# Kernel optimization log

Hardware: AMD Instinct MI355X
Metric: run time of the kernel (lower is better)

## Reference

```python
import jax, jax.numpy as jnp
import numpy as np

B, H, VOCAB, STEPS = 256, 512, 100, 200  # TEXT_MAX_LEN - 1 = 200
SOS_IDX = 0  # char2idx['<SOS>'] == 0 (first entry of chars list)


def setup_inputs() -> dict:
    key = jax.random.key(0)
    ks = jax.random.split(key, 8)
    s = 0.05  # keep gates/tanh away from saturation, like trained-weight scale
    return {
        "feat": jax.random.normal(ks[0], (B, H), jnp.float32),          # resnet pooler_output
        "embed_table": jax.random.normal(ks[1], (VOCAB, H), jnp.float32) * s,
        "w_ih": jax.random.normal(ks[2], (3 * H, H), jnp.float32) * s,   # torch weight_ih_l0
        "w_hh": jax.random.normal(ks[3], (3 * H, H), jnp.float32) * s,   # torch weight_hh_l0
        "b_ih": jax.random.normal(ks[4], (3 * H,), jnp.float32) * s,
        "b_hh": jax.random.normal(ks[5], (3 * H,), jnp.float32) * s,
        "proj_w": jax.random.normal(ks[6], (VOCAB, H), jnp.float32) * s,
        "proj_b": jax.random.normal(ks[7], (VOCAB,), jnp.float32) * s,
    }


def _gru_cell(x, h, w_ih, w_hh, b_ih, b_hh):
    # torch GRU cell: gates ordered [r, z, n]
    gi = x @ w_ih.T + b_ih          # [B, 3H]
    gh = h @ w_hh.T + b_hh          # [B, 3H]
    i_r, i_z, i_n = jnp.split(gi, 3, axis=-1)
    h_r, h_z, h_n = jnp.split(gh, 3, axis=-1)
    r = jax.nn.sigmoid(i_r + h_r)
    z = jax.nn.sigmoid(i_z + h_z)
    n = jnp.tanh(i_n + r * h_n)
    return (1.0 - z) * n + z * h


def reference(feat, embed_table, w_ih, w_hh, b_ih, b_hh, proj_w, proj_b):
    batch = feat.shape[0]
    # hidden initialized from resnet features; first input = embed(<SOS>)
    h0 = feat                                             # [B, H]
    inp0 = jnp.broadcast_to(embed_table[SOS_IDX], (batch, H))

    def step(carry, _):
        inp, h = carry
        h_new = _gru_cell(inp, h, w_ih, w_hh, b_ih, b_hh)
        # GRU output == new hidden (1 layer); it is fed back as next input
        return (h_new, h_new), h_new

    _, outs = jax.lax.scan(step, (inp0, h0), None, length=STEPS)  # [T, B, H]
    res = jnp.transpose(outs, (1, 0, 2))                          # [B, T, H]
    logits = res @ proj_w.T + proj_b                              # [B, T, V]
    return jnp.transpose(logits, (0, 2, 1))                       # [B, V, T]
```

## Files before the change

### kernel.cpp

```cpp
#include <hip/hip_runtime.h>
#include <hip/hip_bf16.h>
#include <math.h>


typedef __bf16 bf16_t;
typedef __bf16 bf16x8 __attribute__((ext_vector_type(8)));
typedef float f32x4 __attribute__((ext_vector_type(4)));
typedef unsigned long long u64;
typedef unsigned short u16;

#define B_ 256
#define H_ 512
#define V_ 100
#define T_ 200
#define NF_ 131072
#define SLAB_ 24576
#define MFMA(a,b,c) __builtin_amdgcn_mfma_f32_16x16x32_bf16((a),(b),(c),0,0,0)

__device__ __forceinline__ float ld_in(const void* p, long i, int isf32) {
    return isf32 ? ((const float*)p)[i] : (float)((const bf16_t*)p)[i];
}

__device__ __forceinline__ bf16_t split_pick(double v, int sp) {
    bf16_t a = (bf16_t)(float)v;
    if (sp == 0) return a;
    double r1 = v - (double)(float)a;
    bf16_t b = (bf16_t)(float)r1;
    if (sp == 1) return b;
    double r2 = r1 - (double)(float)b;
    return (bf16_t)(float)r2;
}

union bfbits { __bf16 b; u16 u; };

__global__ __launch_bounds__(256) void convert_kernel(
    const void* __restrict__ feat, const void* __restrict__ embed,
    const void* __restrict__ wih,  const void* __restrict__ whh,
    const void* __restrict__ bih,  const void* __restrict__ bhh,
    const void* __restrict__ pw,   const void* __restrict__ pb,
    char* __restrict__ barr, int* __restrict__ flag,
    bf16_t* __restrict__ WB, bf16_t* __restrict__ W0, bf16_t* __restrict__ PB,
    bf16_t* __restrict__ hsp, double* __restrict__ hf,
    double* __restrict__ BB, double* __restrict__ pbd, double* __restrict__ gi0)
{
    __shared__ int s_cnt;
    if (threadIdx.x == 0) s_cnt = 0;
    __syncthreads();
    if (threadIdx.x < 128) {
        unsigned w = ((const unsigned*)feat)[threadIdx.x];
        unsigned e = (w >> 7) & 0xFFu;
        if (e >= 0x68u && e <= 0x85u) atomicAdd(&s_cnt, 1);
    }
    __syncthreads();
    const int isf32 = (s_cnt < 96) ? 1 : 0;
    if (blockIdx.x == 0) {
        if (threadIdx.x == 0) *flag = isf32;
        if (threadIdx.x < 16) {
            int g = threadIdx.x & 7;
            int* p = (int*)(barr + ((threadIdx.x < 8) ? (size_t)g * 128
                                                      : 4096 + (size_t)g * 128));
            *p = 0;
        }
    }

    const long S0 = NF_;
    const long S1 = 3145728;
    const long S2 = 2359296;
    const long S3 = 114688;
    const long S4 = 2048;
    const long S5 = 100;
    const long S6 = 1536;
    const long TOT = S0 + S1 + S2 + S3 + S4 + S5 + S6;

    for (long g = blockIdx.x * 256L + threadIdx.x; g < TOT;
         g += (long)gridDim.x * 256L) {
        long i = g;
        if (i < S0) {
            double v = (double)ld_in(feat, i, isf32);
            hf[i] = v;
            hsp[i] = split_pick(v, 0);
            hsp[NF_ + i] = split_pick(v, 1);
            hsp[2 * NF_ + i] = split_pick(v, 2);
            continue;
        }
        i -= S0;
        if (i < S1) {
            long slab = i / SLAB_;  long rem = i % SLAB_;
            int grp = (int)(slab >> 5), jt = (int)(slab & 31);
            int sp = (int)(rem / 8192); long r2 = rem % 8192;
            int c = (int)(r2 / 512), r = (int)((r2 % 512) / 32), kk = (int)(r2 & 31);
            long n = jt * 16 + r, k = c * 32 + kk;
            double v;
            if (grp == 0)      v = (double)ld_in(wih, n * H_ + k, isf32) +
                                   (double)ld_in(whh, n * H_ + k, isf32);
            else if (grp == 1) v = (double)ld_in(wih, (512 + n) * H_ + k, isf32) +
                                   (double)ld_in(whh, (512 + n) * H_ + k, isf32);
            else if (grp == 2) v = (double)ld_in(wih, (1024 + n) * H_ + k, isf32);
            else               v = (double)ld_in(whh, (1024 + n) * H_ + k, isf32);
            WB[i] = split_pick(v, sp);
            continue;
        }
        i -= S1;
        if (i < S2) {
            long slab = i / SLAB_;  long rem = i % SLAB_;
            int grp = (int)(slab >> 5), jt = (int)(slab & 31);
            int sp = (int)(rem / 8192); long r2 = rem % 8192;
            int c = (int)(r2 / 512), r = (int)((r2 % 512) / 32), kk = (int)(r2 & 31);
            long n = jt * 16 + r, k = c * 32 + kk;
            long row = (grp == 0) ? n : (grp == 1) ? (512 + n) : (1024 + n);
            W0[i] = split_pick((double)ld_in(whh, row * H_ + k, isf32), sp);
            continue;
        }
        i -= S2;
        if (i < S3) {
            int vt = (int)(i / 16384); long rem = i % 16384;
            int sp = (int)(rem / 8192); long r2 = rem % 8192;
            int c = (int)(r2 / 512), r = (int)((r2 % 512) / 32), kk = (int)(r2 & 31);
            int v = vt * 16 + r;
            long k = c * 32 + kk;
            double val = (v < V_) ? (double)ld_in(pw, (long)v * H_ + k, isf32) : 0.0;
            PB[i] = split_pick(val, sp);
            continue;
        }
        i -= S3;
        if (i < S4) {
            int grp = (int)(i / 512), j = (int)(i & 511);
            double v;
            if (grp == 0)      v = (double)ld_in(bih, j, isf32) + (double)ld_in(bhh, j, isf32);
            else if (grp == 1) v = (double)ld_in(bih, 512 + j, isf32) + (double)ld_in(bhh, 512 + j, isf32);
            else if (grp == 2) v = (double)ld_in(bih, 1024 + j, isf32);
            else               v = (double)ld_in(bhh, 1024 + j, isf32);
            BB[i] = v;
            continue;
        }
        i -= S4;
        if (i < S5) { pbd[i] = (double)ld_in(pb, i, isf32); continue; }
        i -= S5;
        if (i < S6) {
            double acc = 0.0;
            #pragma unroll 8
            for (int k = 0; k < H_; ++k)
                acc += (double)ld_in(embed, k, isf32) *
                       (double)ld_in(wih, i * H_ + k, isf32);
            gi0[i] = acc;
        }
    }
}

__global__ __launch_bounds__(512, 2) void gru_persist(
    const bf16_t* __restrict__ WB, const bf16_t* __restrict__ W0,
    const bf16_t* __restrict__ PB,
    bf16_t* __restrict__ hsp,
    const double* __restrict__ hf,
    const double* __restrict__ BB, const double* __restrict__ pbd,
    const double* __restrict__ gi0,
    const int* __restrict__ flag, char* __restrict__ barr,
    void* __restrict__ outp)
{
    __shared__ __align__(16) u64 Ad[2][3072];
    __shared__ double Gm[8][32][16];
    __shared__ __align__(16) bf16_t PBl[16384];

    const int tid = threadIdx.x;
    const int w = tid >> 6;
    const int g = w & 3;
    const int par = w >> 2;
    const int lane = tid & 63;
    const int ln = lane & 15;
    const int quad = lane >> 4;
    const int b = blockIdx.x;
    const int x = b & 7;
    const int l = b >> 3;
    const int jt = (x & 3) * 8 + (l & 7);
    const int mh = (x >> 2) * 4 + (l >> 3);
    const int m0base = mh * 32;
    const int isf32 = *flag;

    int* myc = (int*)(barr + (size_t)mh * 128);
    int* mys = (int*)(barr + 4096 + (size_t)mh * 128);

    const int gm = tid >> 4;
    const int gj = tid & 15;
    const int jg = jt * 16 + gj;
    double hreg = hf[(long)(m0base + gm) * H_ + jg];
    const double bbR = BB[jg], bbZ = BB[512 + jg];
    const double bbNI = BB[1024 + jg], bbNH = BB[1536 + jg];
    const double g0R = gi0[jg], g0Z = gi0[512 + jg], g0NI = gi0[1024 + jg];

    bf16x8 Breg[8][3];
    {
        const int gg = (g == 3) ? 2 : g;
        const bf16_t* wpre = W0 + (long)(gg * 32 + jt) * SLAB_ + ln * 32 + quad * 8;
        #pragma unroll
        for (int n = 0; n < 8; ++n)
            #pragma unroll
            for (int sp = 0; sp < 3; ++sp)
                Breg[n][sp] = *(const bf16x8*)(wpre + sp * 8192 + (par + 2 * n) * 512);
    }
    const bf16_t* wpW = WB + (long)(g * 32 + jt) * SLAB_ + ln * 32 + quad * 8;

    const int tpj = jt & 1;

    if (jt < 14) {
        const bf16_t* src = PB + (long)(jt >> 1) * 16384;
        #pragma unroll
        for (int it = 0; it < 4; ++it) {
            int cg = it * 512 + tid;
            int h01 = cg >> 10, c = (cg >> 6) & 15, j = cg & 63;
            int L = (j & 3) * 16 + (j >> 2);
            *(bf16x8*)(PBl + h01 * 8192 + c * 512 + L * 8) =
                *(const bf16x8*)(src + cg * 8);
        }
    }

    const int lf = (((ln ^ quad) ^ ((ln & 1) << 2)) | (quad << 4)) * 8;

    int soff[6]; int ldst[6];
    #pragma unroll
    for (int i = 0; i < 6; ++i) {
        int u = i * 512 + tid;
        int sp = u >> 10, row = (u >> 5) & 31, k64 = u & 31;
        soff[i] = sp * 32768 + (m0base + row) * 128 + k64;
        int lc = k64 >> 3, qd = (k64 & 7) >> 1, half = k64 & 1;
        int lpos = (((row & 15) ^ qd) ^ ((row & 1) << 2)) | (qd << 4);
        ldst[i] = sp * 1024 + lc * 256 + (row >> 4) * 128 + lpos * 2 + half;
    }
    __syncthreads();

    for (int s = 0; s <= T_; ++s) {
        const u64* hin64 = (const u64*)(hsp + (long)(s & 1) * 3 * NF_);
        const bool gemm = (s < T_) && !(s == 0 && g == 2);
        const bool doproj = (s >= 1 && jt < 14 && w == (s & 7));

        double dg0[4] = {0, 0, 0, 0}, dg1[4] = {0, 0, 0, 0};
        f32x4 pacc = {0.f, 0.f, 0.f, 0.f};

        u64 sreg[24];
        #pragma unroll
        for (int qq = 0; qq < 4; ++qq)
            #pragma unroll
            for (int i = 0; i < 6; ++i)
                sreg[qq * 6 + i] = __hip_atomic_load(
                    hin64 + (long)soff[i] + qq * 32,
                    __ATOMIC_RELAXED, __HIP_MEMORY_SCOPE_AGENT);

        #pragma unroll
        for (int i = 0; i < 6; ++i) Ad[0][ldst[i]] = sreg[i];
        __syncthreads();

        #pragma unroll
        for (int q = 0; q < 4; ++q) {
            if (q < 3) {
                #pragma unroll
                for (int i = 0; i < 6; ++i)
                    Ad[(q + 1) & 1][ldst[i]] = sreg[(q + 1) * 6 + i];
            }
            const __bf16* Ab = (const __bf16*)(Ad[q & 1]);

            if (gemm) {
                #pragma unroll
                for (int t = 0; t < 2; ++t) {
                    const int lc = 2 * t + par;
                    const int n = 2 * q + t;
                    bf16x8 A0[3], A1[3];
                    #pragma unroll
                    for (int sp = 0; sp < 3; ++sp) {
                        A0[sp] = *(const bf16x8*)(Ab + sp * 4096 + lc * 1024 + lf);
                        A1[sp] = *(const bf16x8*)(Ab + sp * 4096 + lc * 1024 + 512 + lf);
                    }
                    f32x4 t0 = {0.f, 0.f, 0.f, 0.f};
                    t0 = MFMA(A0[0], Breg[n][2], t0);
                    t0 = MFMA(A0[1], Breg[n][1], t0);
                    t0 = MFMA(A0[2], Breg[n][0], t0);
                    t0 = MFMA(A0[0], Breg[n][1], t0);
                    t0 = MFMA(A0[1], Breg[n][0], t0);
                    t0 = MFMA(A0[0], Breg[n][0], t0);
                    f32x4 t1 = {0.f, 0.f, 0.f, 0.f};
                    t1 = MFMA(A1[0], Breg[n][2], t1);
                    t1 = MFMA(A1[1], Breg[n][1], t1);
                    t1 = MFMA(A1[2], Breg[n][0], t1);
                    t1 = MFMA(A1[0], Breg[n][1], t1);
                    t1 = MFMA(A1[1], Breg[n][0], t1);
                    t1 = MFMA(A1[0], Breg[n][0], t1);
                    #pragma unroll
                    for (int i = 0; i < 4; ++i) {
                        dg0[i] += (double)t0[i];
                        dg1[i] += (double)t1[i];
                    }
                }
            }
            if (doproj) {
                #pragma unroll
                for (int lc = 0; lc < 4; ++lc) {
                    const int c = q * 4 + lc;
                    bf16x8 pa1 = *(const bf16x8*)(Ab + 0 * 4096 + lc * 1024 + tpj * 512 + lf);
                    bf16x8 pa2 = *(const bf16x8*)(Ab + 1 * 4096 + lc * 1024 + tpj * 512 + lf);
                    bf16x8 b1v = *(const bf16x8*)(PBl + c * 512 + lane * 8);
                    bf16x8 b2v = *(const bf16x8*)(PBl + 8192 + c * 512 + lane * 8);
                    pacc = MFMA(pa1, b2v, pacc);
                    pacc = MFMA(pa2, b1v, pacc);
                    pacc = MFMA(pa1, b1v, pacc);
                }
            }
            if (q == 3 && s < T_) {
                #pragma unroll
                for (int i = 0; i < 4; ++i) {
                    Gm[w][quad * 4 + i][ln] = dg0[i];
                    Gm[w][16 + quad * 4 + i][ln] = dg1[i];
                }
            }
            __syncthreads();
        }

        if (doproj) {
            const int v = (jt >> 1) * 16 + ln;
            if (v < V_) {
                const double pbv = pbd[v];
                const int mtp = mh * 2 + tpj;
                #pragma unroll
                for (int i = 0; i < 4; ++i) {
                    const int m = mtp * 16 + quad * 4 + i;
                    const long idx = ((long)m * V_ + v) * T_ + (s - 1);
                    const float val = (float)((double)pacc[i] + pbv);
                    if (isf32) ((float*)outp)[idx] = val;
                    else       ((bf16_t*)outp)[idx] = (bf16_t)val;
                }
            }
        }

        if (s < T_) {
            {
                double R  = Gm[0][gm][gj] + Gm[4][gm][gj] + bbR;
                double Z  = Gm[1][gm][gj] + Gm[5][gm][gj] + bbZ;
                double NI = Gm[2][gm][gj] + Gm[6][gm][gj] + bbNI;
                double NH = Gm[3][gm][gj] + Gm[7][gm][gj] + bbNH;
                if (s == 0) { R += g0R; Z += g0Z; NI += g0NI; }
                const double r = 1.0 / (1.0 + exp(-R));
                const double z = 1.0 / (1.0 + exp(-Z));
                const double pre = NI + r * NH;
                const double n = 1.0 - 2.0 / (exp(2.0 * pre) + 1.0);
                hreg = (1.0 - z) * n + z * hreg;
                const long oi = (long)(m0base + gm) * H_ + jg;
                u16* ho = (u16*)(hsp + (long)((s + 1) & 1) * 3 * NF_);
                bfbits q1, q2, q3;
                q1.b = (bf16_t)(float)hreg;  double r1 = hreg - (double)(float)q1.b;
                q2.b = (bf16_t)(float)r1;    double r2 = r1 - (double)(float)q2.b;
                q3.b = (bf16_t)(float)r2;
                __hip_atomic_store(ho + oi, q1.u, __ATOMIC_RELAXED, __HIP_MEMORY_SCOPE_AGENT);
                __hip_atomic_store(ho + NF_ + oi, q2.u, __ATOMIC_RELAXED, __HIP_MEMORY_SCOPE_AGENT);
                __hip_atomic_store(ho + 2 * NF_ + oi, q3.u, __ATOMIC_RELAXED, __HIP_MEMORY_SCOPE_AGENT);
            }

            __syncthreads();
            if (tid == 0) {
                int old = __hip_atomic_fetch_add(myc, 1, __ATOMIC_RELAXED,
                                                 __HIP_MEMORY_SCOPE_AGENT);
                if (old == 32 * (s + 1) - 1)
                    __hip_atomic_store(mys, s + 1, __ATOMIC_RELAXED,
                                       __HIP_MEMORY_SCOPE_AGENT);
                int lim = 0;
                while (__hip_atomic_load(mys, __ATOMIC_RELAXED,
                                         __HIP_MEMORY_SCOPE_AGENT) < s + 1) {
                    __builtin_amdgcn_s_sleep(2);
                    if (++lim > 100000000) break;
                }
            }
            __syncthreads();
            if (s == 0) {
                #pragma unroll
                for (int n = 0; n < 8; ++n)
                    #pragma unroll
                    for (int sp = 0; sp < 3; ++sp)
                        Breg[n][sp] = *(const bf16x8*)(wpW + sp * 8192 + (par + 2 * n) * 512);
            }
        }
    }
}

extern "C" void kernel_launch(void* const* d_in, const int* in_sizes, int n_in,
                              void* d_out, int out_size, void* d_ws, size_t ws_size,
                              hipStream_t stream) {
    char* ws = (char*)d_ws;
    char*   barr = ws;
    int*    flag = (int*)(ws + 8192);
    bf16_t* WB  = (bf16_t*)(ws + 8448);
    bf16_t* W0  = (bf16_t*)(ws + 6299904);
    bf16_t* PB  = (bf16_t*)(ws + 11018496);
    bf16_t* hsp = (bf16_t*)(ws + 11477248);
    double* hf  = (double*)(ws + 13050112);
    double* BB  = (double*)(ws + 15147264);
    double* pbd = (double*)(ws + 15163648);
    double* gi0 = (double*)(ws + 15164672);

    convert_kernel<<<1024, 256, 0, stream>>>(
        d_in[0], d_in[1], d_in[2], d_in[3], d_in[4], d_in[5], d_in[6], d_in[7],
        barr, flag, WB, W0, PB, hsp, hf, BB, pbd, gi0);

    gru_persist<<<256, 512, 0, stream>>>(
        WB, W0, PB, hsp, hf, BB, pbd, gi0, flag, barr, d_out);
}
```

Baseline: 1.474 ms.

## Dedicate wave 7 to projection, stage h with seven waves, add LDS swizzle/padding

The per-step staging of the hidden-state slab from global memory into LDS is now split across waves 0-6 only (seven loads per thread with a tail guard), and wave 7 always does the output projection instead of rotating that job across waves by step. The LDS layout of the A tile gets an extra XOR swizzle keyed on the k-chunk, and the Gm reduction buffer is padded from 16 to 18 columns to cut bank conflicts. The aim is to take the load latency off the projecting wave and to reduce LDS conflicts. The cost is more staging work per thread in the other waves and imbalance, since wave 7 carries the projection MFMAs every step.

```diff
diff --git a/kernel.cpp b/kernel.cpp
--- a/kernel.cpp
+++ b/kernel.cpp
@@ -158,7 +158,7 @@
     void* __restrict__ outp)
 {
     __shared__ __align__(16) u64 Ad[2][3072];
-    __shared__ double Gm[8][32][16];
+    __shared__ double Gm[8][32][18];
     __shared__ __align__(16) bf16_t PBl[16384];
 
     const int tid = threadIdx.x;
@@ -215,45 +215,51 @@
 
     const int lf = (((ln ^ quad) ^ ((ln & 1) << 2)) | (quad << 4)) * 8;
 
-    int soff[6]; int ldst[6];
+    const bool stager = (w < 7);
+    int soff[7]; int ldst[7];
     #pragma unroll
-    for (int i = 0; i < 6; ++i) {
-        int u = i * 512 + tid;
+    for (int k = 0; k < 7; ++k) {
+        int u = k * 448 + tid;
         int sp = u >> 10, row = (u >> 5) & 31, k64 = u & 31;
-        soff[i] = sp * 32768 + (m0base + row) * 128 + k64;
+        soff[k] = sp * 32768 + (m0base + row) * 128 + k64;
         int lc = k64 >> 3, qd = (k64 & 7) >> 1, half = k64 & 1;
-        int lpos = (((row & 15) ^ qd) ^ ((row & 1) << 2)) | (qd << 4);
-        ldst[i] = sp * 1024 + lc * 256 + (row >> 4) * 128 + lpos * 2 + half;
+        int lpos = ((((row & 15) ^ qd) ^ ((row & 1) << 2)) ^ (lc << 1)) | (qd << 4);
+        ldst[k] = sp * 1024 + lc * 256 + (row >> 4) * 128 + lpos * 2 + half;
     }
     __syncthreads();
 
     for (int s = 0; s <= T_; ++s) {
         const u64* hin64 = (const u64*)(hsp + (long)(s & 1) * 3 * NF_);
         const bool gemm = (s < T_) && !(s == 0 && g == 2);
-        const bool doproj = (s >= 1 && jt < 14 && w == (s & 7));
+        const bool doproj = (s >= 1 && jt < 14 && w == 7);
 
         double dg0[4] = {0, 0, 0, 0}, dg1[4] = {0, 0, 0, 0};
         f32x4 pacc = {0.f, 0.f, 0.f, 0.f};
 
-        u64 sreg[24];
-        #pragma unroll
-        for (int qq = 0; qq < 4; ++qq)
+        u64 sreg[28];
+        if (stager) {
             #pragma unroll
-            for (int i = 0; i < 6; ++i)
-                sreg[qq * 6 + i] = __hip_atomic_load(
-                    hin64 + (long)soff[i] + qq * 32,
-                    __ATOMIC_RELAXED, __HIP_MEMORY_SCOPE_AGENT);
-
-        #pragma unroll
-        for (int i = 0; i < 6; ++i) Ad[0][ldst[i]] = sreg[i];
+            for (int qq = 0; qq < 4; ++qq)
+                #pragma unroll
+                for (int k = 0; k < 7; ++k)
+                    if (k < 6 || tid < 384)
+                        sreg[qq * 7 + k] = __hip_atomic_load(
+                            hin64 + (long)soff[k] + qq * 32,
+                            __ATOMIC_RELAXED, __HIP_MEMORY_SCOPE_AGENT);
+
+            #pragma unroll
+            for (int k = 0; k < 7; ++k)
+                if (k < 6 || tid < 384) Ad[0][ldst[k]] = sreg[k];
+        }
         __syncthreads();
 
         #pragma unroll
         for (int q = 0; q < 4; ++q) {
-            if (q < 3) {
-                #pragma unroll
-                for (int i = 0; i < 6; ++i)
-                    Ad[(q + 1) & 1][ldst[i]] = sreg[(q + 1) * 6 + i];
+            if (q < 3 && stager) {
+                #pragma unroll
+                for (int k = 0; k < 7; ++k)
+                    if (k < 6 || tid < 384)
+                        Ad[(q + 1) & 1][ldst[k]] = sreg[(q + 1) * 7 + k];
             }
             const __bf16* Ab = (const __bf16*)(Ad[q & 1]);
 
@@ -262,11 +268,12 @@
                 for (int t = 0; t < 2; ++t) {
                     const int lc = 2 * t + par;
                     const int n = 2 * q + t;
+                    const int lfa = lf ^ (lc << 4);
                     bf16x8 A0[3], A1[3];
                     #pragma unroll
                     for (int sp = 0; sp < 3; ++sp) {
-                        A0[sp] = *(const bf16x8*)(Ab + sp * 4096 + lc * 1024 + lf);
-                        A1[sp] = *(const bf16x8*)(Ab + sp * 4096 + lc * 1024 + 512 + lf);
+                        A0[sp] = *(const bf16x8*)(Ab + sp * 4096 + lc * 1024 + lfa);
+                        A1[sp] = *(const bf16x8*)(Ab + sp * 4096 + lc * 1024 + 512 + lfa);
                     }
                     f32x4 t0 = {0.f, 0.f, 0.f, 0.f};
                     t0 = MFMA(A0[0], Breg[n][2], t0);
@@ -293,8 +300,9 @@
                 #pragma unroll
                 for (int lc = 0; lc < 4; ++lc) {
                     const int c = q * 4 + lc;
-                    bf16x8 pa1 = *(const bf16x8*)(Ab + 0 * 4096 + lc * 1024 + tpj * 512 + lf);
-                    bf16x8 pa2 = *(const bf16x8*)(Ab + 1 * 4096 + lc * 1024 + tpj * 512 + lf);
+                    const int lfa = lf ^ (lc << 4);
+                    bf16x8 pa1 = *(const bf16x8*)(Ab + 0 * 4096 + lc * 1024 + tpj * 512 + lfa);
+                    bf16x8 pa2 = *(const bf16x8*)(Ab + 1 * 4096 + lc * 1024 + tpj * 512 + lfa);
                     bf16x8 b1v = *(const bf16x8*)(PBl + c * 512 + lane * 8);
                     bf16x8 b2v = *(const bf16x8*)(PBl + 8192 + c * 512 + lane * 8);
                     pacc = MFMA(pa1, b2v, pacc);
```

After: 1.521 ms. 3.2% more time.

## Split batch tiles to 16 rows and double persistent grid to 512 blocks

Applied to the files above, without the earlier changes.

Halves the batch rows each persistent block handles (32 to 16) and doubles the grid to 512 blocks, raising launch bounds occupancy to 4 blocks per SM. The goal is more CUs working on each recurrent step and a shorter per-step critical path. Barrier counters grow from 8 to 16 groups, and half the threads now sit idle in the gate update phase. The risk is that every block still holds the full weight slab in registers, so register pressure rises and more blocks take part in each barrier.

```diff
diff --git a/kernel.cpp b/kernel.cpp
--- a/kernel.cpp
+++ b/kernel.cpp
@@ -55,10 +55,10 @@
     const int isf32 = (s_cnt < 96) ? 1 : 0;
     if (blockIdx.x == 0) {
         if (threadIdx.x == 0) *flag = isf32;
-        if (threadIdx.x < 16) {
-            int g = threadIdx.x & 7;
-            int* p = (int*)(barr + ((threadIdx.x < 8) ? (size_t)g * 128
-                                                      : 4096 + (size_t)g * 128));
+        if (threadIdx.x < 32) {
+            int i = threadIdx.x;
+            int* p = (int*)(barr + ((i < 16) ? (size_t)i * 128
+                                             : 4096 + (size_t)(i - 16) * 128));
             *p = 0;
         }
     }
@@ -147,7 +147,7 @@
     }
 }
 
-__global__ __launch_bounds__(512, 2) void gru_persist(
+__global__ __launch_bounds__(512, 4) void gru_persist(
     const bf16_t* __restrict__ WB, const bf16_t* __restrict__ W0,
     const bf16_t* __restrict__ PB,
     bf16_t* __restrict__ hsp,
@@ -157,8 +157,8 @@
     const int* __restrict__ flag, char* __restrict__ barr,
     void* __restrict__ outp)
 {
-    __shared__ __align__(16) u64 Ad[2][3072];
-    __shared__ double Gm[8][32][16];
+    __shared__ __align__(16) u64 Ad[2][1536];
+    __shared__ double Gm[8][16][16];
     __shared__ __align__(16) bf16_t PBl[16384];
 
     const int tid = threadIdx.x;
@@ -172,8 +172,8 @@
     const int x = b & 7;
     const int l = b >> 3;
     const int jt = (x & 3) * 8 + (l & 7);
-    const int mh = (x >> 2) * 4 + (l >> 3);
-    const int m0base = mh * 32;
+    const int mh = (x >> 2) * 8 + (l >> 3);
+    const int m0base = mh * 16;
     const int isf32 = *flag;
 
     int* myc = (int*)(barr + (size_t)mh * 128);
@@ -182,7 +182,8 @@
     const int gm = tid >> 4;
     const int gj = tid & 15;
     const int jg = jt * 16 + gj;
-    double hreg = hf[(long)(m0base + gm) * H_ + jg];
+    double hreg = 0.0;
+    if (tid < 256) hreg = hf[(long)(m0base + gm) * H_ + jg];
     const double bbR = BB[jg], bbZ = BB[512 + jg];
     const double bbNI = BB[1024 + jg], bbNH = BB[1536 + jg];
     const double g0R = gi0[jg], g0Z = gi0[512 + jg], g0NI = gi0[1024 + jg];
@@ -199,10 +200,8 @@
     }
     const bf16_t* wpW = WB + (long)(g * 32 + jt) * SLAB_ + ln * 32 + quad * 8;
 
-    const int tpj = jt & 1;
-
-    if (jt < 14) {
-        const bf16_t* src = PB + (long)(jt >> 1) * 16384;
+    if (jt < 7) {
+        const bf16_t* src = PB + (long)jt * 16384;
         #pragma unroll
         for (int it = 0; it < 4; ++it) {
             int cg = it * 512 + tid;
@@ -215,45 +214,45 @@
 
     const int lf = (((ln ^ quad) ^ ((ln & 1) << 2)) | (quad << 4)) * 8;
 
-    int soff[6]; int ldst[6];
+    int soff[3]; int ldst[3];
     #pragma unroll
-    for (int i = 0; i < 6; ++i) {
+    for (int i = 0; i < 3; ++i) {
         int u = i * 512 + tid;
-        int sp = u >> 10, row = (u >> 5) & 31, k64 = u & 31;
+        int sp = u >> 9, row = (u >> 5) & 15, k64 = u & 31;
         soff[i] = sp * 32768 + (m0base + row) * 128 + k64;
         int lc = k64 >> 3, qd = (k64 & 7) >> 1, half = k64 & 1;
         int lpos = (((row & 15) ^ qd) ^ ((row & 1) << 2)) | (qd << 4);
-        ldst[i] = sp * 1024 + lc * 256 + (row >> 4) * 128 + lpos * 2 + half;
+        ldst[i] = sp * 512 + lc * 128 + lpos * 2 + half;
     }
     __syncthreads();
 
     for (int s = 0; s <= T_; ++s) {
         const u64* hin64 = (const u64*)(hsp + (long)(s & 1) * 3 * NF_);
         const bool gemm = (s < T_) && !(s == 0 && g == 2);
-        const bool doproj = (s >= 1 && jt < 14 && w == (s & 7));
-
-        double dg0[4] = {0, 0, 0, 0}, dg1[4] = {0, 0, 0, 0};
+        const bool doproj = (s >= 1 && jt < 7 && w == (s & 7));
+
+        double dg0[4] = {0, 0, 0, 0};
         f32x4 pacc = {0.f, 0.f, 0.f, 0.f};
 
-        u64 sreg[24];
+        u64 sreg[12];
         #pragma unroll
         for (int qq = 0; qq < 4; ++qq)
             #pragma unroll
-            for (int i = 0; i < 6; ++i)
-                sreg[qq * 6 + i] = __hip_atomic_load(
+            for (int i = 0; i < 3; ++i)
+                sreg[qq * 3 + i] = __hip_atomic_load(
                     hin64 + (long)soff[i] + qq * 32,
                     __ATOMIC_RELAXED, __HIP_MEMORY_SCOPE_AGENT);
 
         #pragma unroll
-        for (int i = 0; i < 6; ++i) Ad[0][ldst[i]] = sreg[i];
+        for (int i = 0; i < 3; ++i) Ad[0][ldst[i]] = sreg[i];
         __syncthreads();
 
         #pragma unroll
         for (int q = 0; q < 4; ++q) {
             if (q < 3) {
                 #pragma unroll
-                for (int i = 0; i < 6; ++i)
-                    Ad[(q + 1) & 1][ldst[i]] = sreg[(q + 1) * 6 + i];
+                for (int i = 0; i < 3; ++i)
+                    Ad[(q + 1) & 1][ldst[i]] = sreg[(q + 1) * 3 + i];
             }
             const __bf16* Ab = (const __bf16*)(Ad[q & 1]);
 
@@ -262,12 +261,10 @@
                 for (int t = 0; t < 2; ++t) {
                     const int lc = 2 * t + par;
                     const int n = 2 * q + t;
-                    bf16x8 A0[3], A1[3];
+                    bf16x8 A0[3];
                     #pragma unroll
-                    for (int sp = 0; sp < 3; ++sp) {
-                        A0[sp] = *(const bf16x8*)(Ab + sp * 4096 + lc * 1024 + lf);
-                        A1[sp] = *(const bf16x8*)(Ab + sp * 4096 + lc * 1024 + 512 + lf);
-                    }
+                    for (int sp = 0; sp < 3; ++sp)
+                        A0[sp] = *(const bf16x8*)(Ab + sp * 2048 + lc * 512 + lf);
                     f32x4 t0 = {0.f, 0.f, 0.f, 0.f};
                     t0 = MFMA(A0[0], Breg[n][2], t0);
                     t0 = MFMA(A0[1], Breg[n][1], t0);
@@ -275,26 +272,16 @@
                     t0 = MFMA(A0[0], Breg[n][1], t0);
                     t0 = MFMA(A0[1], Breg[n][0], t0);
                     t0 = MFMA(A0[0], Breg[n][0], t0);
-                    f32x4 t1 = {0.f, 0.f, 0.f, 0.f};
-                    t1 = MFMA(A1[0], Breg[n][2], t1);
-                    t1 = MFMA(A1[1], Breg[n][1], t1);
-                    t1 = MFMA(A1[2], Breg[n][0], t1);
-                    t1 = MFMA(A1[0], Breg[n][1], t1);
-                    t1 = MFMA(A1[1], Breg[n][0], t1);
-                    t1 = MFMA(A1[0], Breg[n][0], t1);
                     #pragma unroll
-                    for (int i = 0; i < 4; ++i) {
-                        dg0[i] += (double)t0[i];
-                        dg1[i] += (double)t1[i];
-                    }
+                    for (int i = 0; i < 4; ++i) dg0[i] += (double)t0[i];
                 }
             }
             if (doproj) {
                 #pragma unroll
                 for (int lc = 0; lc < 4; ++lc) {
                     const int c = q * 4 + lc;
-                    bf16x8 pa1 = *(const bf16x8*)(Ab + 0 * 4096 + lc * 1024 + tpj * 512 + lf);
-                    bf16x8 pa2 = *(const bf16x8*)(Ab + 1 * 4096 + lc * 1024 + tpj * 512 + lf);
+                    bf16x8 pa1 = *(const bf16x8*)(Ab + 0 * 2048 + lc * 512 + lf);
+                    bf16x8 pa2 = *(const bf16x8*)(Ab + 1 * 2048 + lc * 512 + lf);
                     bf16x8 b1v = *(const bf16x8*)(PBl + c * 512 + lane * 8);
                     bf16x8 b2v = *(const bf16x8*)(PBl + 8192 + c * 512 + lane * 8);
                     pacc = MFMA(pa1, b2v, pacc);
@@ -304,22 +291,19 @@
             }
             if (q == 3 && s < T_) {
                 #pragma unroll
-                for (int i = 0; i < 4; ++i) {
+                for (int i = 0; i < 4; ++i)
                     Gm[w][quad * 4 + i][ln] = dg0[i];
-                    Gm[w][16 + quad * 4 + i][ln] = dg1[i];
-                }
             }
             __syncthreads();
         }
 
         if (doproj) {
-            const int v = (jt >> 1) * 16 + ln;
+            const int v = jt * 16 + ln;
             if (v < V_) {
                 const double pbv = pbd[v];
-                const int mtp = mh * 2 + tpj;
                 #pragma unroll
                 for (int i = 0; i < 4; ++i) {
-                    const int m = mtp * 16 + quad * 4 + i;
+                    const int m = m0base + quad * 4 + i;
                     const long idx = ((long)m * V_ + v) * T_ + (s - 1);
                     const float val = (float)((double)pacc[i] + pbv);
                     if (isf32) ((float*)outp)[idx] = val;
@@ -329,7 +313,7 @@
         }
 
         if (s < T_) {
-            {
+            if (tid < 256) {
                 double R  = Gm[0][gm][gj] + Gm[4][gm][gj] + bbR;
                 double Z  = Gm[1][gm][gj] + Gm[5][gm][gj] + bbZ;
                 double NI = Gm[2][gm][gj] + Gm[6][gm][gj] + bbNI;
@@ -396,6 +380,6 @@
         d_in[0], d_in[1], d_in[2], d_in[3], d_in[4], d_in[5], d_in[6], d_in[7],
         barr, flag, WB, W0, PB, hsp, hf, BB, pbd, gi0);
 
-    gru_persist<<<256, 512, 0, stream>>>(
+    gru_persist<<<512, 512, 0, stream>>>(
         WB, W0, PB, hsp, hf, BB, pbd, gi0, flag, barr, d_out);
 }
```

Result: slower. 2.616 ms (+77.5%).
